# Performance work log

Measured on AMD Instinct MI355X. Metric: run time of the kernel, lower is better.

## Reference

```python
import jax, jax.numpy as jnp
import numpy as np

N_NODES = 50000
N_EDGES = 500000
H = 128
C = 2


def setup_inputs() -> dict:
    key = jax.random.key(0)
    ks = jax.random.split(key, 8)
    node_repr = jax.random.normal(ks[0], (N_NODES, H), dtype=jnp.float32)
    src = jax.random.randint(ks[1], (N_EDGES,), 0, N_NODES, dtype=jnp.int32)
    dst = jax.random.randint(ks[2], (N_EDGES,), 0, N_NODES, dtype=jnp.int32)
    # Linear weights stored as (in, out); scaled like torch default init
    W1 = jax.random.normal(ks[3], (4 * H, 2 * H), dtype=jnp.float32) / np.sqrt(4 * H)
    b1 = jnp.zeros((2 * H,), dtype=jnp.float32)
    W2 = jax.random.normal(ks[4], (2 * H, H), dtype=jnp.float32) / np.sqrt(2 * H)
    b2 = jnp.zeros((H,), dtype=jnp.float32)
    W3 = jax.random.normal(ks[5], (H, C), dtype=jnp.float32) / np.sqrt(H)
    b3 = jnp.zeros((C,), dtype=jnp.float32)
    return {"node_repr": node_repr, "src": src, "dst": dst,
            "W1": W1, "b1": b1, "W2": W2, "b2": b2, "W3": W3, "b3": b3}


def reference(node_repr, src, dst, W1, b1, W2, b2, W3, b3):
    h_i = node_repr[src]                      # [E, H] gather
    h_j = node_repr[dst]                      # [E, H] gather
    diff = jnp.abs(h_i - h_j)
    product = h_i * h_j
    edge_input = jnp.concatenate([h_i, h_j, diff, product], axis=1)  # [E, 4H]
    x = jax.nn.relu(edge_input @ W1 + b1)     # [E, 2H]; dropout = identity (eval)
    x = jax.nn.relu(x @ W2 + b2)              # [E, H]
    return x @ W3 + b3                        # [E, C]
```

## Files before the change

### kernel.cpp

```cpp
#include <hip/hip_runtime.h>


#define H 128

typedef __bf16 bf16x8 __attribute__((ext_vector_type(8)));
typedef float f32x4 __attribute__((ext_vector_type(4)));

__device__ __forceinline__ unsigned short f2bf(float f) {
    unsigned u = __builtin_bit_cast(unsigned, f);
    u += 0x7FFFu + ((u >> 16) & 1u);
    return (unsigned short)(u >> 16);
}
__device__ __forceinline__ float bfhi(unsigned u) {
    return __builtin_bit_cast(float, u & 0xffff0000u);
}
__device__ __forceinline__ float bflo(unsigned u) {
    return __builtin_bit_cast(float, u << 16);
}
__device__ __forceinline__ unsigned pk2(float r0, float r1) {
    unsigned u0 = __builtin_bit_cast(unsigned, r0) + 0x8000u;
    unsigned u1 = __builtin_bit_cast(unsigned, r1) + 0x8000u;
    return __builtin_amdgcn_perm(u1, u0, 0x07060302u);
}
__device__ __forceinline__ unsigned comb(unsigned ua, unsigned ub, bool isdiff) {
    float a0 = bflo(ua), a1 = bfhi(ua);
    float b0 = bflo(ub), b1 = bfhi(ub);
    float r0 = isdiff ? fabsf(a0 - b0) : a0 * b0;
    float r1 = isdiff ? fabsf(a1 - b1) : a1 * b1;
    return pk2(r0, r1);
}
__device__ __forceinline__ unsigned short cvt1(float v) {
    unsigned u = __builtin_bit_cast(unsigned, v) + 0x8000u;
    return (unsigned short)(u >> 16);
}

__global__ void prep_node(const float* __restrict__ node, unsigned short* __restrict__ nbf) {
    int idx = blockIdx.x * 256 + threadIdx.x;
    const f32x4* p = (const f32x4*)(node) + idx;
    f32x4 v = *p;
    ushort4 w;
    w.x = f2bf(v.x); w.y = f2bf(v.y); w.z = f2bf(v.z); w.w = f2bf(v.w);
    *(ushort4*)(nbf + idx * 4) = w;
}

__global__ void prep_w1(const float* __restrict__ W1, unsigned short* __restrict__ W1P) {
    int o = blockIdx.x * 256 + threadIdx.x;
    int chunk = o >> 9;
    int g_nt = chunk >> 4;
    int ks = chunk & 15;
    int r = o & 511;
    int lane = r >> 3;
    int j = r & 7;
    int row = g_nt * 16 + (lane & 15);
    int k = ks * 32 + (lane >> 4) * 8 + j;
    W1P[o] = f2bf(W1[k * 256 + row]);
}

__global__ void prep_w2(const float* __restrict__ W2, unsigned short* __restrict__ W2P) {
    int o = blockIdx.x * 256 + threadIdx.x;
    int chunk = o >> 9;
    int g_nt = chunk >> 3;
    int ks = chunk & 7;
    int r = o & 511;
    int lane = r >> 3;
    int j = r & 7;
    int row = g_nt * 16 + (lane & 15);
    int k = ks * 32 + (lane >> 4) * 8 + j;
    W2P[o] = f2bf(W2[k * 128 + row]);
}

__launch_bounds__(256, 4)
__global__ void fused_mlp(const unsigned short* __restrict__ nbf,
                          const int* __restrict__ src,
                          const int* __restrict__ dst,
                          const unsigned short* __restrict__ W1P,
                          const float* __restrict__ b1,
                          const unsigned short* __restrict__ W2P,
                          const float* __restrict__ b2,
                          const float* __restrict__ W3,
                          const float* __restrict__ b3,
                          float* __restrict__ out,
                          int E) {
    __shared__ __align__(16) unsigned short sH[64 * 268];
    __shared__ __align__(16) float sW3[256];

    const int t = threadIdx.x;
    const int e0 = blockIdx.x * 64;

    const int lane = t & 63;
    const int wv = t >> 6;
    const int quad = lane >> 4;
    const int lrow = lane & 15;
    const int nb = wv * 64;
    const int nb2 = wv * 32;

    const unsigned short* w1b = W1P + wv * 32768 + lane * 8;
    const unsigned short* w2b = W2P + wv * 8192 + lane * 8;

    {
        int r = t >> 2;
        int q = t & 3;
        int e = e0 + r;
        int ec = e < E ? e : (E - 1);
        const unsigned short* hi = nbf + (long)src[ec] * H + q * 32;
        const unsigned short* hj = nbf + (long)dst[ec] * H + q * 32;
        unsigned short* rowp = sH + r * 268 + q * 32;
#pragma unroll
        for (int b = 0; b < 4; b++) {
            uint4 a = *(const uint4*)(hi + b * 8);
            uint4 c = *(const uint4*)(hj + b * 8);
            *(uint4*)(rowp + b * 8)       = a;
            *(uint4*)(rowp + 136 + b * 8) = c;
        }
        sW3[(t & 1) * 128 + (t >> 1)] = W3[t];
    }
    __syncthreads();

    f32x4 acc[4][4];
#pragma unroll
    for (int mt = 0; mt < 4; mt++)
#pragma unroll
        for (int nt = 0; nt < 4; nt++)
            acc[mt][nt] = (f32x4){0.f, 0.f, 0.f, 0.f};

    int aoff[4];
#pragma unroll
    for (int mt = 0; mt < 4; mt++) aoff[mt] = (mt * 16 + lrow) * 268 + quad * 8;

#pragma unroll 1
    for (int ks = 0; ks < 8; ks++) {
        const int ao = (ks < 4) ? ks * 32 : 136 + (ks - 4) * 32;
        bf16x8 bv[4], av[4];
#pragma unroll
        for (int nt = 0; nt < 4; nt++) bv[nt] = *(const bf16x8*)(w1b + nt * 8192 + ks * 512);
#pragma unroll
        for (int mt = 0; mt < 4; mt++) av[mt] = *(const bf16x8*)(sH + aoff[mt] + ao);
#pragma unroll
        for (int mt = 0; mt < 4; mt++)
#pragma unroll
            for (int nt = 0; nt < 4; nt++)
                acc[mt][nt] = __builtin_amdgcn_mfma_f32_16x16x32_bf16(av[mt], bv[nt], acc[mt][nt], 0, 0, 0);
    }

    float b1v[4];
#pragma unroll
    for (int nt = 0; nt < 4; nt++) b1v[nt] = b1[nb + nt * 16 + lrow];

    __syncthreads();

    {
        int r = t >> 2;
        int c0 = (t & 3) * 32;
        unsigned short* rowp = sH + r * 268;
#pragma unroll
        for (int j = 0; j < 4; j++) {
            uint4 ua = *(const uint4*)(rowp + c0 + j * 8);
            uint4 ub = *(const uint4*)(rowp + 136 + c0 + j * 8);
            uint4 dd, pp;
            dd.x = comb(ua.x, ub.x, true);  dd.y = comb(ua.y, ub.y, true);
            dd.z = comb(ua.z, ub.z, true);  dd.w = comb(ua.w, ub.w, true);
            pp.x = comb(ua.x, ub.x, false); pp.y = comb(ua.y, ub.y, false);
            pp.z = comb(ua.z, ub.z, false); pp.w = comb(ua.w, ub.w, false);
            *(uint2*)(rowp + c0 + j * 8)           = (uint2){dd.x, dd.y};
            *(uint2*)(rowp + c0 + j * 8 + 4)       = (uint2){dd.z, dd.w};
            *(uint2*)(rowp + 136 + c0 + j * 8)     = (uint2){pp.x, pp.y};
            *(uint2*)(rowp + 136 + c0 + j * 8 + 4) = (uint2){pp.z, pp.w};
        }
    }
    __syncthreads();

#pragma unroll 1
    for (int ks = 0; ks < 8; ks++) {
        const int ao = (ks < 4) ? ks * 32 : 136 + (ks - 4) * 32;
        bf16x8 bv[4], av[4];
#pragma unroll
        for (int nt = 0; nt < 4; nt++) bv[nt] = *(const bf16x8*)(w1b + nt * 8192 + (ks + 8) * 512);
#pragma unroll
        for (int mt = 0; mt < 4; mt++) av[mt] = *(const bf16x8*)(sH + aoff[mt] + ao);
#pragma unroll
        for (int mt = 0; mt < 4; mt++)
#pragma unroll
            for (int nt = 0; nt < 4; nt++)
                acc[mt][nt] = __builtin_amdgcn_mfma_f32_16x16x32_bf16(av[mt], bv[nt], acc[mt][nt], 0, 0, 0);
    }

    float b2v[2];
#pragma unroll
    for (int nt = 0; nt < 2; nt++) b2v[nt] = b2[nb2 + nt * 16 + lrow];

    __syncthreads();
    unsigned short* sx1 = sH;
#pragma unroll
    for (int mt = 0; mt < 4; mt++)
#pragma unroll
        for (int nt = 0; nt < 4; nt++)
#pragma unroll
            for (int i = 0; i < 4; i++) {
                int row = mt * 16 + quad * 4 + i;
                int col = nb + nt * 16 + lrow;
                float v = acc[mt][nt][i] + b1v[nt];
                v = v > 0.f ? v : 0.f;
                sx1[row * 268 + col] = cvt1(v);
            }
    __syncthreads();

    f32x4 acc2[4][2];
#pragma unroll
    for (int mt = 0; mt < 4; mt++)
#pragma unroll
        for (int nt = 0; nt < 2; nt++)
            acc2[mt][nt] = (f32x4){0.f, 0.f, 0.f, 0.f};

#pragma unroll 1
    for (int ks = 0; ks < 8; ks++) {
        bf16x8 bv2[2], av2[4];
#pragma unroll
        for (int nt = 0; nt < 2; nt++) bv2[nt] = *(const bf16x8*)(w2b + nt * 4096 + ks * 512);
#pragma unroll
        for (int mt = 0; mt < 4; mt++) av2[mt] = *(const bf16x8*)(sx1 + aoff[mt] + ks * 32);
#pragma unroll
        for (int mt = 0; mt < 4; mt++)
#pragma unroll
            for (int nt = 0; nt < 2; nt++)
                acc2[mt][nt] = __builtin_amdgcn_mfma_f32_16x16x32_bf16(av2[mt], bv2[nt], acc2[mt][nt], 0, 0, 0);
    }

    __syncthreads();
    unsigned short* sx2 = sH;
#pragma unroll
    for (int mt = 0; mt < 4; mt++)
#pragma unroll
        for (int nt = 0; nt < 2; nt++)
#pragma unroll
            for (int i = 0; i < 4; i++) {
                int row = mt * 16 + quad * 4 + i;
                int col = nb2 + nt * 16 + lrow;
                float v = acc2[mt][nt][i] + b2v[nt];
                v = v > 0.f ? v : 0.f;
                sx2[row * 140 + col] = cvt1(v);
            }
    __syncthreads();

    {
        int r = t >> 2;
        int c = t & 1;
        int h = (t >> 1) & 1;
        const unsigned short* xr = sx2 + r * 140 + h * 64;
        const float* w3c = sW3 + c * 128 + h * 64;
        float s = 0.f;
#pragma unroll
        for (int j = 0; j < 8; j++) {
            uint4 v = *(const uint4*)(xr + j * 8);
            const float* w = w3c + j * 8;
            s += bflo(v.x) * w[0] + bfhi(v.x) * w[1]
               + bflo(v.y) * w[2] + bfhi(v.y) * w[3]
               + bflo(v.z) * w[4] + bfhi(v.z) * w[5]
               + bflo(v.w) * w[6] + bfhi(v.w) * w[7];
        }
        s += __shfl_xor(s, 2);
        int e = e0 + r;
        if (h == 0 && e < E) out[e * 2 + c] = s + b3[c];
    }
}

extern "C" void kernel_launch(void* const* d_in, const int* in_sizes, int n_in,
                              void* d_out, int out_size, void* d_ws, size_t ws_size,
                              hipStream_t stream) {
    const float* node = (const float*)d_in[0];
    const int* src    = (const int*)d_in[1];
    const int* dst    = (const int*)d_in[2];
    const float* W1   = (const float*)d_in[3];
    const float* b1   = (const float*)d_in[4];
    const float* W2   = (const float*)d_in[5];
    const float* b2   = (const float*)d_in[6];
    const float* W3   = (const float*)d_in[7];
    const float* b3   = (const float*)d_in[8];
    float* out = (float*)d_out;
    const int NN = in_sizes[0] / H;
    const int E = in_sizes[1];

    unsigned short* W1P = (unsigned short*)d_ws;
    unsigned short* W2P = W1P + 512 * 256;
    unsigned short* NBF = W2P + 256 * 128;

    hipLaunchKernelGGL(prep_node, dim3((NN * H / 4 + 255) / 256), dim3(256), 0, stream, node, NBF);
    hipLaunchKernelGGL(prep_w1, dim3(512), dim3(256), 0, stream, W1, W1P);
    hipLaunchKernelGGL(prep_w2, dim3(128), dim3(256), 0, stream, W2, W2P);
    const int nblk = (E + 63) / 64;
    hipLaunchKernelGGL(fused_mlp, dim3(nblk), dim3(256), 0, stream,
                       NBF, src, dst, W1P, b1, W2P, b2, W3, b3, out, E);
}
```

Measured before the change: 382.6 us.

## Double edge tile to 128 rows per block to reuse weight fragments

Each block now processes 128 edges instead of 64, so every wave runs 8 M-tiles per weight fragment loaded from global memory. This halves the number of W1/W2 fragment loads per edge and doubles MFMA work per B-fragment. In exchange, accumulator registers double (128 floats for acc), launch bounds drop to 2 blocks per CU, and LDS use doubles to about 69KB per block, which lowers occupancy and the ability to hide gather latency. The final W3 dot product now uses one thread per (edge, class) with no shuffle.

```diff
diff --git a/kernel.cpp b/kernel.cpp
--- a/kernel.cpp
+++ b/kernel.cpp
@@ -69,7 +69,7 @@
     W2P[o] = f2bf(W2[k * 128 + row]);
 }
 
-__launch_bounds__(256, 4)
+__launch_bounds__(256, 2)
 __global__ void fused_mlp(const unsigned short* __restrict__ nbf,
                           const int* __restrict__ src,
                           const int* __restrict__ dst,
@@ -81,11 +81,11 @@
                           const float* __restrict__ b3,
                           float* __restrict__ out,
                           int E) {
-    __shared__ __align__(16) unsigned short sH[64 * 268];
+    __shared__ __align__(16) unsigned short sH[128 * 268];
     __shared__ __align__(16) float sW3[256];
 
     const int t = threadIdx.x;
-    const int e0 = blockIdx.x * 64;
+    const int e0 = blockIdx.x * 128;
 
     const int lane = t & 63;
     const int wv = t >> 6;
@@ -98,15 +98,15 @@
     const unsigned short* w2b = W2P + wv * 8192 + lane * 8;
 
     {
-        int r = t >> 2;
-        int q = t & 3;
+        int r = t >> 1;
+        int q = t & 1;
         int e = e0 + r;
         int ec = e < E ? e : (E - 1);
-        const unsigned short* hi = nbf + (long)src[ec] * H + q * 32;
-        const unsigned short* hj = nbf + (long)dst[ec] * H + q * 32;
-        unsigned short* rowp = sH + r * 268 + q * 32;
-#pragma unroll
-        for (int b = 0; b < 4; b++) {
+        const unsigned short* hi = nbf + (long)src[ec] * H + q * 64;
+        const unsigned short* hj = nbf + (long)dst[ec] * H + q * 64;
+        unsigned short* rowp = sH + r * 268 + q * 64;
+#pragma unroll
+        for (int b = 0; b < 8; b++) {
             uint4 a = *(const uint4*)(hi + b * 8);
             uint4 c = *(const uint4*)(hj + b * 8);
             *(uint4*)(rowp + b * 8)       = a;
@@ -116,30 +116,30 @@
     }
     __syncthreads();
 
-    f32x4 acc[4][4];
-#pragma unroll
-    for (int mt = 0; mt < 4; mt++)
+    f32x4 acc[8][4];
+#pragma unroll
+    for (int mt = 0; mt < 8; mt++)
 #pragma unroll
         for (int nt = 0; nt < 4; nt++)
             acc[mt][nt] = (f32x4){0.f, 0.f, 0.f, 0.f};
 
-    int aoff[4];
-#pragma unroll
-    for (int mt = 0; mt < 4; mt++) aoff[mt] = (mt * 16 + lrow) * 268 + quad * 8;
+    int aoff[8];
+#pragma unroll
+    for (int mt = 0; mt < 8; mt++) aoff[mt] = (mt * 16 + lrow) * 268 + quad * 8;
 
 #pragma unroll 1
     for (int ks = 0; ks < 8; ks++) {
         const int ao = (ks < 4) ? ks * 32 : 136 + (ks - 4) * 32;
-        bf16x8 bv[4], av[4];
+        bf16x8 bv[4];
 #pragma unroll
         for (int nt = 0; nt < 4; nt++) bv[nt] = *(const bf16x8*)(w1b + nt * 8192 + ks * 512);
 #pragma unroll
-        for (int mt = 0; mt < 4; mt++) av[mt] = *(const bf16x8*)(sH + aoff[mt] + ao);
-#pragma unroll
-        for (int mt = 0; mt < 4; mt++)
+        for (int mt = 0; mt < 8; mt++) {
+            bf16x8 av = *(const bf16x8*)(sH + aoff[mt] + ao);
 #pragma unroll
             for (int nt = 0; nt < 4; nt++)
-                acc[mt][nt] = __builtin_amdgcn_mfma_f32_16x16x32_bf16(av[mt], bv[nt], acc[mt][nt], 0, 0, 0);
+                acc[mt][nt] = __builtin_amdgcn_mfma_f32_16x16x32_bf16(av, bv[nt], acc[mt][nt], 0, 0, 0);
+        }
     }
 
     float b1v[4];
@@ -149,11 +149,11 @@
     __syncthreads();
 
     {
-        int r = t >> 2;
-        int c0 = (t & 3) * 32;
+        int r = t >> 1;
+        int c0 = (t & 1) * 64;
         unsigned short* rowp = sH + r * 268;
 #pragma unroll
-        for (int j = 0; j < 4; j++) {
+        for (int j = 0; j < 8; j++) {
             uint4 ua = *(const uint4*)(rowp + c0 + j * 8);
             uint4 ub = *(const uint4*)(rowp + 136 + c0 + j * 8);
             uint4 dd, pp;
@@ -172,16 +172,16 @@
 #pragma unroll 1
     for (int ks = 0; ks < 8; ks++) {
         const int ao = (ks < 4) ? ks * 32 : 136 + (ks - 4) * 32;
-        bf16x8 bv[4], av[4];
+        bf16x8 bv[4];
 #pragma unroll
         for (int nt = 0; nt < 4; nt++) bv[nt] = *(const bf16x8*)(w1b + nt * 8192 + (ks + 8) * 512);
 #pragma unroll
-        for (int mt = 0; mt < 4; mt++) av[mt] = *(const bf16x8*)(sH + aoff[mt] + ao);
-#pragma unroll
-        for (int mt = 0; mt < 4; mt++)
+        for (int mt = 0; mt < 8; mt++) {
+            bf16x8 av = *(const bf16x8*)(sH + aoff[mt] + ao);
 #pragma unroll
             for (int nt = 0; nt < 4; nt++)
-                acc[mt][nt] = __builtin_amdgcn_mfma_f32_16x16x32_bf16(av[mt], bv[nt], acc[mt][nt], 0, 0, 0);
+                acc[mt][nt] = __builtin_amdgcn_mfma_f32_16x16x32_bf16(av, bv[nt], acc[mt][nt], 0, 0, 0);
+        }
     }
 
     float b2v[2];
@@ -191,7 +191,7 @@
     __syncthreads();
     unsigned short* sx1 = sH;
 #pragma unroll
-    for (int mt = 0; mt < 4; mt++)
+    for (int mt = 0; mt < 8; mt++)
 #pragma unroll
         for (int nt = 0; nt < 4; nt++)
 #pragma unroll
@@ -204,31 +204,31 @@
             }
     __syncthreads();
 
-    f32x4 acc2[4][2];
-#pragma unroll
-    for (int mt = 0; mt < 4; mt++)
+    f32x4 acc2[8][2];
+#pragma unroll
+    for (int mt = 0; mt < 8; mt++)
 #pragma unroll
         for (int nt = 0; nt < 2; nt++)
             acc2[mt][nt] = (f32x4){0.f, 0.f, 0.f, 0.f};
 
 #pragma unroll 1
     for (int ks = 0; ks < 8; ks++) {
-        bf16x8 bv2[2], av2[4];
+        bf16x8 bv2[2];
 #pragma unroll
         for (int nt = 0; nt < 2; nt++) bv2[nt] = *(const bf16x8*)(w2b + nt * 4096 + ks * 512);
 #pragma unroll
-        for (int mt = 0; mt < 4; mt++) av2[mt] = *(const bf16x8*)(sx1 + aoff[mt] + ks * 32);
-#pragma unroll
-        for (int mt = 0; mt < 4; mt++)
+        for (int mt = 0; mt < 8; mt++) {
+            bf16x8 av2 = *(const bf16x8*)(sx1 + aoff[mt] + ks * 32);
 #pragma unroll
             for (int nt = 0; nt < 2; nt++)
-                acc2[mt][nt] = __builtin_amdgcn_mfma_f32_16x16x32_bf16(av2[mt], bv2[nt], acc2[mt][nt], 0, 0, 0);
+                acc2[mt][nt] = __builtin_amdgcn_mfma_f32_16x16x32_bf16(av2, bv2[nt], acc2[mt][nt], 0, 0, 0);
+        }
     }
 
     __syncthreads();
     unsigned short* sx2 = sH;
 #pragma unroll
-    for (int mt = 0; mt < 4; mt++)
+    for (int mt = 0; mt < 8; mt++)
 #pragma unroll
         for (int nt = 0; nt < 2; nt++)
 #pragma unroll
@@ -242,14 +242,13 @@
     __syncthreads();
 
     {
-        int r = t >> 2;
+        int r = t >> 1;
         int c = t & 1;
-        int h = (t >> 1) & 1;
-        const unsigned short* xr = sx2 + r * 140 + h * 64;
-        const float* w3c = sW3 + c * 128 + h * 64;
+        const unsigned short* xr = sx2 + r * 140;
+        const float* w3c = sW3 + c * 128;
         float s = 0.f;
 #pragma unroll
-        for (int j = 0; j < 8; j++) {
+        for (int j = 0; j < 16; j++) {
             uint4 v = *(const uint4*)(xr + j * 8);
             const float* w = w3c + j * 8;
             s += bflo(v.x) * w[0] + bfhi(v.x) * w[1]
@@ -257,9 +256,8 @@
                + bflo(v.z) * w[4] + bfhi(v.z) * w[5]
                + bflo(v.w) * w[6] + bfhi(v.w) * w[7];
         }
-        s += __shfl_xor(s, 2);
         int e = e0 + r;
-        if (h == 0 && e < E) out[e * 2 + c] = s + b3[c];
+        if (e < E) out[e * 2 + c] = s + b3[c];
     }
 }
 
@@ -286,7 +284,7 @@
     hipLaunchKernelGGL(prep_node, dim3((NN * H / 4 + 255) / 256), dim3(256), 0, stream, node, NBF);
     hipLaunchKernelGGL(prep_w1, dim3(512), dim3(256), 0, stream, W1, W1P);
     hipLaunchKernelGGL(prep_w2, dim3(128), dim3(256), 0, stream, W2, W2P);
-    const int nblk = (E + 63) / 64;
+    const int nblk = (E + 127) / 128;
     hipLaunchKernelGGL(fused_mlp, dim3(nblk), dim3(256), 0, stream,
                        NBF, src, dst, W1P, b1, W2P, b2, W3, b3, out, E);
 }
```

Result: slower. 412.0 us (+7.7%).
